# Kernel optimization log

Hardware: AMD Instinct MI355X
Metric: run time of the kernel (lower is better)

The kernel has to match this reference:

```python
import jax, jax.numpy as jnp
import numpy as np

B, S, D, L, H = 4, 2048, 1024, 2, 8  # batch, seq, d_model, hierarchy levels, heads
DH = D // H


def _ln(x, g, b, eps=1e-5):
    mu = jnp.mean(x, axis=-1, keepdims=True)
    xc = x - mu
    var = jnp.mean(xc * xc, axis=-1, keepdims=True)
    return xc * jax.lax.rsqrt(var + eps) * g + b


def setup_inputs() -> dict:
    key = jax.random.key(0)
    ks = jax.random.split(key, 16)
    s = 0.02
    f32 = jnp.float32
    return {
        "x": jax.random.normal(ks[0], (B, S, D), f32),
        "hierarchy_levels": jax.random.randint(ks[1], (B, S), 0, 3),
        # per-level processor MLPs (stacked over level axis)
        "p1_w": jax.random.normal(ks[2], (L, D, D), f32) * s,
        "p1_b": jnp.zeros((L, D), f32),
        "p2_w": jax.random.normal(ks[3], (L, D, D), f32) * s,
        "p2_b": jnp.zeros((L, D), f32),
        "ln_g": jnp.ones((L, D), f32),
        "ln_b": jnp.zeros((L, D), f32),
        # multihead attention projections
        "wq": jax.random.normal(ks[4], (D, D), f32) * s,
        "bq": jnp.zeros((D,), f32),
        "wk": jax.random.normal(ks[5], (D, D), f32) * s,
        "bk": jnp.zeros((D,), f32),
        "wv": jax.random.normal(ks[6], (D, D), f32) * s,
        "bv": jnp.zeros((D,), f32),
        "wo": jax.random.normal(ks[7], (D, D), f32) * s,
        "bo": jnp.zeros((D,), f32),
        # integration MLP: Linear(L*D -> D), SiLU, Linear(D -> D), LayerNorm
        "i1_w": jax.random.normal(ks[8], (L * D, D), f32) * s,
        "i1_b": jnp.zeros((D,), f32),
        "i2_w": jax.random.normal(ks[9], (D, D), f32) * s,
        "i2_b": jnp.zeros((D,), f32),
        "iln_g": jnp.ones((D,), f32),
        "iln_b": jnp.zeros((D,), f32),
    }


def reference(x, hierarchy_levels, p1_w, p1_b, p2_w, p2_b, ln_g, ln_b,
              wq, bq, wk, bk, wv, bv, wo, bo,
              i1_w, i1_b, i2_w, i2_b, iln_g, iln_b):
    # --- per-token expert routing: compute all L processors, select by level ---
    t = jax.nn.silu(jnp.einsum('bsd,lde->lbse', x, p1_w) + p1_b[:, None, None, :])
    h = jnp.einsum('lbse,led->lbsd', t, p2_w) + p2_b[:, None, None, :]
    h = _ln(h, ln_g[:, None, None, :], ln_b[:, None, None, :])  # [L,B,S,D]
    oh = jax.nn.one_hot(hierarchy_levels, L, dtype=x.dtype)      # [B,S,L]; level>=L -> all-zero row
    hsel = jnp.einsum('lbsd,bsl->bsd', h, oh)                    # [B,S,D]
    # --- self-attention over routed outputs ---
    q = (hsel @ wq + bq).reshape(B, S, H, DH)
    k = (hsel @ wk + bk).reshape(B, S, H, DH)
    v = (hsel @ wv + bv).reshape(B, S, H, DH)
    scores = jnp.einsum('bqhd,bkhd->bhqk', q, k) / np.sqrt(DH).astype(x.dtype)
    a = jax.nn.softmax(scores, axis=-1)                          # [B,H,S,S]
    ctx = jnp.einsum('bhqk,bkhd->bqhd', a, v).reshape(B, S, D)
    attended = ctx @ wo + bo
    attn_weights = jnp.mean(a, axis=1)                           # torch avg over heads: [B,S,S]
    # --- integration MLP ---
    z = jnp.concatenate([hsel, attended], axis=-1)               # [B,S,2D]
    z = jax.nn.silu(z @ i1_w + i1_b) @ i2_w + i2_b
    out = _ln(z, iln_g, iln_b)
    return out, attn_weights
```

## Files before the change

kernel.cpp:

```cpp
#include <hip/hip_runtime.h>
#include <cstdint>
#include <cstddef>

#define B_ 4
#define S_ 2048
#define D_ 1024
#define H_ 8
#define DH_ 128
#define MTOT 8192
#define NT_ 32
#define SCALE2 (0.08838834764831845f * 1.4426950408889634f)

typedef __attribute__((ext_vector_type(8))) short s16x8;
typedef __attribute__((ext_vector_type(4))) float f32x4;
typedef __attribute__((ext_vector_type(8))) __bf16 bf16x8;

static __device__ __forceinline__ f32x4 mfma16(s16x8 a, s16x8 b, f32x4 c) {
  return __builtin_amdgcn_mfma_f32_16x16x32_bf16(
      __builtin_bit_cast(bf16x8, a), __builtin_bit_cast(bf16x8, b), c, 0, 0, 0);
}
static __device__ __forceinline__ unsigned short f2bf(float f) {
  unsigned u = __builtin_bit_cast(unsigned, f);
  u += 0x7fffu + ((u >> 16) & 1u);
  return (unsigned short)(u >> 16);
}
static __device__ __forceinline__ unsigned cvtpk2(float a, float b) {
  unsigned r;
  asm("v_cvt_pk_bf16_f32 %0, %1, %2" : "=v"(r) : "v"(a), "v"(b));
  return r;
}
static __device__ __forceinline__ void gload_lds16(const void* g, void* l) {
  __builtin_amdgcn_global_load_lds(
      (__attribute__((address_space(1))) void*)(void*)(g),
      (__attribute__((address_space(3))) void*)(l), 16, 0, 0);
}

__global__ __launch_bounds__(256) void xconv_kernel(const float* __restrict__ x,
                                                    unsigned short* __restrict__ xb) {
  long i = ((long)blockIdx.x * 256 + threadIdx.x) * 4;
  float4 v = *(const float4*)(x + i);
  ushort4 o;
  o.x = f2bf(v.x); o.y = f2bf(v.y); o.z = f2bf(v.z); o.w = f2bf(v.w);
  *(ushort4*)(xb + i) = o;
}

__global__ __launch_bounds__(256) void route_kernel(const int* __restrict__ levels,
                                                    int* __restrict__ cnt,
                                                    int* __restrict__ ridx) {
  int row = blockIdx.x * 256 + threadIdx.x;
  int lvl = levels[row];
  if (lvl < 2) {
    int slot = atomicAdd(&cnt[lvl], 1);
    ridx[lvl * MTOT + slot] = row;
  }
}

__global__ __launch_bounds__(256) void wtrans_kernel(const float* __restrict__ in,
                                                     unsigned short* __restrict__ out,
                                                     int R, int C) {
  __shared__ unsigned short tile[32][33];
  int r0 = blockIdx.y * 32, c0 = blockIdx.x * 32;
  int tr = threadIdx.x >> 5, tc = threadIdx.x & 31;
#pragma unroll
  for (int i = 0; i < 4; i++)
    tile[tr + i * 8][tc] = f2bf(in[(long)(r0 + tr + i * 8) * C + c0 + tc]);
  __syncthreads();
#pragma unroll
  for (int i = 0; i < 4; i++)
    out[(long)(c0 + tr + i * 8) * R + r0 + tc] = tile[tc][tr + i * 8];
}

__global__ __launch_bounds__(256) void vtrans_kernel(const unsigned short* __restrict__ V,
                                                     unsigned short* __restrict__ Vt) {
  __shared__ unsigned short tile[32][33];
  int b = blockIdx.z;
  int h = blockIdx.y >> 2, d0 = (blockIdx.y & 3) * 32;
  int s0 = blockIdx.x * 32;
  int tr = threadIdx.x >> 5, tc = threadIdx.x & 31;
#pragma unroll
  for (int i = 0; i < 4; i++)
    tile[tr + i * 8][tc] = V[((long)(b * S_) + s0 + tr + i * 8) * D_ + h * DH_ + d0 + tc];
  __syncthreads();
  const int sk = s0 + tc;
  const int k6 = sk & 63;
  const int slot = ((k6 >> 5) << 5) | (((k6 >> 2) & 3) << 3) | (((k6 >> 4) & 1) << 2) | (k6 & 3);
  const int ss = (sk & ~63) | slot;
#pragma unroll
  for (int i = 0; i < 4; i++)
    Vt[((long)(b * H_ + h) * DH_ + d0 + tr + i * 8) * S_ + ss] = tile[tc][tr + i * 8];
}

template <int TAG>
__global__ __launch_bounds__(256) void gemm_kernel(
    const unsigned short* __restrict__ A, int lda,
    const unsigned short* __restrict__ Wt, int ldw,
    const float* __restrict__ bias, float oscale,
    unsigned short* __restrict__ Cb, float* __restrict__ Cf, int ldc,
    int K, int do_silu) {
  __shared__ unsigned short lA[128 * 64];
  __shared__ unsigned short lB[128 * 64];
  const int t = threadIdx.x;
  const int wid = t >> 6, lane = t & 63;
  const int g = lane >> 4, lc = lane & 15;
  const int wr = wid >> 1, wc = wid & 1;
  const int nwg = gridDim.x * gridDim.y;
  int flat = blockIdx.x + gridDim.x * blockIdx.y;
  flat = (flat & 7) * (nwg >> 3) + (flat >> 3);
  const int m0 = (flat / gridDim.x) * 128;
  const int n0 = (flat % gridDim.x) * 128;
  const int srow = lane >> 3, scol = lane & 7;
  const int sxor = (scol ^ srow) << 4;

  f32x4 acc[4][4];
#pragma unroll
  for (int i = 0; i < 4; i++)
#pragma unroll
    for (int j = 0; j < 4; j++) acc[i][j] = (f32x4){0.f, 0.f, 0.f, 0.f};

  const int nk = K >> 6;
  for (int kt = 0; kt < nk; ++kt) {
    const int k0 = kt << 6;
#pragma unroll
    for (int i = 0; i < 4; i++) {
      const int r0 = wid * 32 + i * 8;
      gload_lds16((const char*)(A + (m0 + r0 + srow) * (long)lda + k0) + sxor,
                  (char*)lA + r0 * 128);
      gload_lds16((const char*)(Wt + (n0 + r0 + srow) * (long)ldw + k0) + sxor,
                  (char*)lB + r0 * 128);
    }
    __syncthreads();
#pragma unroll
    for (int kk = 0; kk < 2; kk++) {
      s16x8 af[4], bfr[4];
#pragma unroll
      for (int i = 0; i < 4; i++) {
        int row = wr * 64 + i * 16 + lc;
        af[i] = *(const s16x8*)((const char*)lA + row * 128 +
                                ((kk * 64 + g * 16) ^ ((row & 7) << 4)));
      }
#pragma unroll
      for (int j = 0; j < 4; j++) {
        int row = wc * 64 + j * 16 + lc;
        bfr[j] = *(const s16x8*)((const char*)lB + row * 128 +
                                 ((kk * 64 + g * 16) ^ ((row & 7) << 4)));
      }
#pragma unroll
      for (int i = 0; i < 4; i++)
#pragma unroll
        for (int j = 0; j < 4; j++) acc[i][j] = mfma16(af[i], bfr[j], acc[i][j]);
    }
    __syncthreads();
  }
#pragma unroll
  for (int i = 0; i < 4; i++) {
    const long rbase = m0 + wr * 64 + i * 16 + g * 4;
#pragma unroll
    for (int j = 0; j < 4; j++) {
      const int col = n0 + wc * 64 + j * 16 + lc;
      const float bv = bias[col];
#pragma unroll
      for (int r = 0; r < 4; r++) {
        float v = (acc[i][j][r] + bv) * oscale;
        if (do_silu) v = v / (1.f + __expf(-v));
        if (Cb) Cb[(rbase + r) * (long)ldc + col] = f2bf(v);
        else Cf[(rbase + r) * (long)ldc + col] = v;
      }
    }
  }
}

template <int RMAP>
__global__ __launch_bounds__(256) void gemm_moe_kernel(
    const unsigned short* __restrict__ A, int lda,
    const unsigned short* __restrict__ Wt0, int ldw,
    const float* __restrict__ bias0,
    unsigned short* __restrict__ Cb, float* __restrict__ Cf, int ldc,
    int K, int do_silu, const int* __restrict__ ridx, const int* __restrict__ cnt2) {
  __shared__ unsigned short lA[128 * 64];
  __shared__ unsigned short lB[128 * 64];
  const int t = threadIdx.x;
  const int wid = t >> 6, lane = t & 63;
  const int g = lane >> 4, lc = lane & 15;
  const int wr = wid >> 1, wc = wid & 1;
  const int nwg = gridDim.x * gridDim.y;
  int flat = blockIdx.x + gridDim.x * blockIdx.y;
  flat = (flat & 7) * (nwg >> 3) + (flat >> 3);
  const int m0 = (flat / gridDim.x) * 128;
  const int n0 = (flat % gridDim.x) * 128;
  const int lvl = m0 >> 12;
  const int lm0 = m0 & 4095;
  if (lm0 >= cnt2[lvl]) return;
  const unsigned short* Wt = Wt0 + (long)lvl * 1048576;
  const float* bias = bias0 + lvl * 1024;
  const int srow = lane >> 3, scol = lane & 7;
  const int sxor = (scol ^ srow) << 4;

  const unsigned short* abase[4];
#pragma unroll
  for (int i = 0; i < 4; i++) {
    int ar;
    if (RMAP) ar = ridx[lvl * MTOT + lm0 + wid * 32 + i * 8 + srow];
    else ar = m0 + wid * 32 + i * 8 + srow;
    abase[i] = A + (long)ar * lda;
  }

  f32x4 acc[4][4];
#pragma unroll
  for (int i = 0; i < 4; i++)
#pragma unroll
    for (int j = 0; j < 4; j++) acc[i][j] = (f32x4){0.f, 0.f, 0.f, 0.f};

  const int nk = K >> 6;
  for (int kt = 0; kt < nk; ++kt) {
    const int k0 = kt << 6;
#pragma unroll
    for (int i = 0; i < 4; i++) {
      const int r0 = wid * 32 + i * 8;
      gload_lds16((const char*)(abase[i] + k0) + sxor, (char*)lA + r0 * 128);
      gload_lds16((const char*)(Wt + (n0 + r0 + srow) * (long)ldw + k0) + sxor,
                  (char*)lB + r0 * 128);
    }
    __syncthreads();
#pragma unroll
    for (int kk = 0; kk < 2; kk++) {
      s16x8 af[4], bfr[4];
#pragma unroll
      for (int i = 0; i < 4; i++) {
        int row = wr * 64 + i * 16 + lc;
        af[i] = *(const s16x8*)((const char*)lA + row * 128 +
                                ((kk * 64 + g * 16) ^ ((row & 7) << 4)));
      }
#pragma unroll
      for (int j = 0; j < 4; j++) {
        int row = wc * 64 + j * 16 + lc;
        bfr[j] = *(const s16x8*)((const char*)lB + row * 128 +
                                 ((kk * 64 + g * 16) ^ ((row & 7) << 4)));
      }
#pragma unroll
      for (int i = 0; i < 4; i++)
#pragma unroll
        for (int j = 0; j < 4; j++) acc[i][j] = mfma16(af[i], bfr[j], acc[i][j]);
    }
    __syncthreads();
  }
#pragma unroll
  for (int i = 0; i < 4; i++) {
    const long rbase = m0 + wr * 64 + i * 16 + g * 4;
#pragma unroll
    for (int j = 0; j < 4; j++) {
      const int col = n0 + wc * 64 + j * 16 + lc;
      const float bv = bias[col];
#pragma unroll
      for (int r = 0; r < 4; r++) {
        float v = acc[i][j][r] + bv;
        if (do_silu) v = v / (1.f + __expf(-v));
        if (Cb) Cb[(rbase + r) * (long)ldc + col] = f2bf(v);
        else Cf[(rbase + r) * (long)ldc + col] = v;
      }
    }
  }
}

__global__ __launch_bounds__(256) void ln_moe_kernel(
    const float* __restrict__ in, const int* __restrict__ ridx,
    const int* __restrict__ cnt2,
    const float* __restrict__ gg0, const float* __restrict__ bb0,
    unsigned short* __restrict__ outb, long ldo) {
  const int row = blockIdx.x;
  const int lvl = row >> 12;
  const int lrow = row & 4095;
  if (lrow >= cnt2[lvl]) return;
  const int orow = ridx[lvl * MTOT + lrow];
  const float* gg = gg0 + lvl * 1024;
  const float* bb = bb0 + lvl * 1024;
  const int t = threadIdx.x;
  const float4 v = *(const float4*)(in + (long)row * D_ + t * 4);
  float s1 = v.x + v.y + v.z + v.w;
  float s2 = v.x * v.x + v.y * v.y + v.z * v.z + v.w * v.w;
#pragma unroll
  for (int m = 32; m; m >>= 1) {
    s1 += __shfl_xor(s1, m);
    s2 += __shfl_xor(s2, m);
  }
  __shared__ float w1[4], w2[4];
  if ((t & 63) == 0) { w1[t >> 6] = s1; w2[t >> 6] = s2; }
  __syncthreads();
  s1 = w1[0] + w1[1] + w1[2] + w1[3];
  s2 = w2[0] + w2[1] + w2[2] + w2[3];
  const float mu = s1 * (1.f / D_);
  const float var = s2 * (1.f / D_) - mu * mu;
  const float rs = rsqrtf(var + 1e-5f);
#pragma unroll
  for (int jj = 0; jj < 4; jj++) {
    int col = t * 4 + jj;
    float xv = (jj == 0 ? v.x : jj == 1 ? v.y : jj == 2 ? v.z : v.w);
    float y = (xv - mu) * rs * gg[col] + bb[col];
    outb[(long)orow * ldo + col] = f2bf(y);
  }
}

__global__ __launch_bounds__(256) void ln_kernel(
    const float* __restrict__ in,
    const float* __restrict__ gg, const float* __restrict__ bb,
    float* __restrict__ outf) {
  const int row = blockIdx.x;
  const int t = threadIdx.x;
  const float4 v = *(const float4*)(in + (long)row * D_ + t * 4);
  float s1 = v.x + v.y + v.z + v.w;
  float s2 = v.x * v.x + v.y * v.y + v.z * v.z + v.w * v.w;
#pragma unroll
  for (int m = 32; m; m >>= 1) {
    s1 += __shfl_xor(s1, m);
    s2 += __shfl_xor(s2, m);
  }
  __shared__ float w1[4], w2[4];
  if ((t & 63) == 0) { w1[t >> 6] = s1; w2[t >> 6] = s2; }
  __syncthreads();
  s1 = w1[0] + w1[1] + w1[2] + w1[3];
  s2 = w2[0] + w2[1] + w2[2] + w2[3];
  const float mu = s1 * (1.f / D_);
  const float var = s2 * (1.f / D_) - mu * mu;
  const float rs = rsqrtf(var + 1e-5f);
#pragma unroll
  for (int jj = 0; jj < 4; jj++) {
    int col = t * 4 + jj;
    float xv = (jj == 0 ? v.x : jj == 1 ? v.y : jj == 2 ? v.z : v.w);
    outf[(long)row * D_ + col] = (xv - mu) * rs * gg[col] + bb[col];
  }
}

__global__ __launch_bounds__(256) void gemm_qkv_kernel(
    const unsigned short* __restrict__ A, int lda,
    const unsigned short* __restrict__ Wt,
    const float* __restrict__ bq, const float* __restrict__ bk,
    const float* __restrict__ bv,
    unsigned short* __restrict__ qb, unsigned short* __restrict__ kb,
    unsigned short* __restrict__ vb) {
  __shared__ unsigned short lA[128 * 64];
  __shared__ unsigned short lB[128 * 64];
  const int t = threadIdx.x;
  const int wid = t >> 6, lane = t & 63;
  const int g = lane >> 4, lc = lane & 15;
  const int wr = wid >> 1, wc = wid & 1;
  const int nwg = gridDim.x * gridDim.y;
  int flat = blockIdx.x + gridDim.x * blockIdx.y;
  flat = (flat & 7) * (nwg >> 3) + (flat >> 3);
  const int m0 = (flat / gridDim.x) * 128;
  const int n0 = (flat % gridDim.x) * 128;
  const int srow = lane >> 3, scol = lane & 7;
  const int sxor = (scol ^ srow) << 4;

  f32x4 acc[4][4];
#pragma unroll
  for (int i = 0; i < 4; i++)
#pragma unroll
    for (int j = 0; j < 4; j++) acc[i][j] = (f32x4){0.f, 0.f, 0.f, 0.f};

  for (int kt = 0; kt < 16; ++kt) {
    const int k0 = kt << 6;
#pragma unroll
    for (int i = 0; i < 4; i++) {
      const int r0 = wid * 32 + i * 8;
      gload_lds16((const char*)(A + (m0 + r0 + srow) * (long)lda + k0) + sxor,
                  (char*)lA + r0 * 128);
      gload_lds16((const char*)(Wt + (n0 + r0 + srow) * 1024 + k0) + sxor,
                  (char*)lB + r0 * 128);
    }
    __syncthreads();
#pragma unroll
    for (int kk = 0; kk < 2; kk++) {
      s16x8 af[4], bfr[4];
#pragma unroll
      for (int i = 0; i < 4; i++) {
        int row = wr * 64 + i * 16 + lc;
        af[i] = *(const s16x8*)((const char*)lA + row * 128 +
                                ((kk * 64 + g * 16) ^ ((row & 7) << 4)));
      }
#pragma unroll
      for (int j = 0; j < 4; j++) {
        int row = wc * 64 + j * 16 + lc;
        bfr[j] = *(const s16x8*)((const char*)lB + row * 128 +
                                 ((kk * 64 + g * 16) ^ ((row & 7) << 4)));
      }
#pragma unroll
      for (int i = 0; i < 4; i++)
#pragma unroll
        for (int j = 0; j < 4; j++) acc[i][j] = mfma16(af[i], bfr[j], acc[i][j]);
    }
    __syncthreads();
  }
  const int whichB = n0 >> 10;
  const float* bias = whichB == 0 ? bq : whichB == 1 ? bk : bv;
  unsigned short* Cb = whichB == 0 ? qb : whichB == 1 ? kb : vb;
  const float oscale = whichB == 0 ? (float)SCALE2 : 1.0f;
  const int nb = n0 & 1023;
#pragma unroll
  for (int i = 0; i < 4; i++) {
    const long rbase = m0 + wr * 64 + i * 16 + g * 4;
#pragma unroll
    for (int j = 0; j < 4; j++) {
      const int col = nb + wc * 64 + j * 16 + lc;
      const float bvv = bias[col];
#pragma unroll
      for (int r = 0; r < 4; r++) {
        float v = (acc[i][j][r] + bvv) * oscale;
        Cb[(rbase + r) * 1024L + col] = f2bf(v);
      }
    }
  }
}

__global__ __launch_bounds__(256, 2) void flash_kernel(
    const unsigned short* __restrict__ Q, const unsigned short* __restrict__ Kb,
    const unsigned short* __restrict__ Vt,
    unsigned short* __restrict__ ctx, float* __restrict__ Mo, float* __restrict__ Lo) {
  __shared__ unsigned short lK[2][64 * 128];
  __shared__ unsigned short lV[2][128 * 64];
  const int t = threadIdx.x, wid = t >> 6, lane = t & 63;
  const int g = lane >> 4, lc = lane & 15;
  const int d = blockIdx.x + 16 * (blockIdx.y + 8 * blockIdx.z);
  const int qd = d >> 3, rd = d & 7;
  const int grp = rd + 8 * (qd >> 4);
  const int b = grp >> 3, h = grp & 7, q0 = (qd & 15) * 128;
  const int k_l4 = lane >> 4, k_c = lane & 15;
  const int v_l3 = lane >> 3, v_c = lane & 7;

  s16x8 qf[2][4];
#pragma unroll
  for (int qi = 0; qi < 2; qi++)
#pragma unroll
    for (int kk = 0; kk < 4; kk++)
      qf[qi][kk] = *(const s16x8*)(Q +
          ((long)(b * S_ + q0 + wid * 32 + qi * 16 + lc)) * D_ + h * DH_ + kk * 32 + g * 8);

  f32x4 acco[2][8];
#pragma unroll
  for (int qi = 0; qi < 2; qi++)
#pragma unroll
    for (int dn = 0; dn < 8; dn++) acco[qi][dn] = (f32x4){0.f, 0.f, 0.f, 0.f};
  float m_run[2] = {-1e30f, -1e30f}, l_run[2] = {0.f, 0.f};

  auto stageK = [&](int kt, int buf) {
#pragma unroll
    for (int i = 0; i < 4; i++) {
      const int r0 = wid * 16 + i * 4;
      const int row = r0 + k_l4;
      gload_lds16((const char*)(Kb + (b * S_ + kt * 64 + row) * D_ + h * DH_) +
                      ((k_c ^ (row & 7)) << 4),
                  (char*)&lK[buf][0] + r0 * 256);
    }
  };
  auto stageV = [&](int kt, int buf) {
#pragma unroll
    for (int i = 0; i < 4; i++) {
      const int r0 = wid * 32 + i * 8;
      const int row = r0 + v_l3;
      gload_lds16((const char*)(Vt + ((b * H_ + h) * DH_ + row) * S_ + kt * 64) +
                      ((v_c ^ (row & 7)) << 4),
                  (char*)&lV[buf][0] + r0 * 128);
    }
  };

  stageK(0, 0);
  stageV(0, 0);
  __syncthreads();

  for (int kt = 0; kt < NT_; ++kt) {
    const int cur = kt & 1;
    if (kt + 1 < NT_) { stageK(kt + 1, cur ^ 1); stageV(kt + 1, cur ^ 1); }

    f32x4 s[2][4];
#pragma unroll
    for (int qi = 0; qi < 2; qi++)
#pragma unroll
      for (int kn = 0; kn < 4; kn++) s[qi][kn] = (f32x4){0.f, 0.f, 0.f, 0.f};
    __builtin_amdgcn_s_setprio(1);
#pragma unroll
    for (int kk = 0; kk < 4; kk++) {
      s16x8 kf[4];
#pragma unroll
      for (int kn = 0; kn < 4; kn++) {
        int row = kn * 16 + lc;
        kf[kn] = *(const s16x8*)((const char*)&lK[cur][0] + row * 256 +
                                 ((kk * 64 + g * 16) ^ ((row & 7) << 4)));
      }
#pragma unroll
      for (int qi = 0; qi < 2; qi++)
#pragma unroll
        for (int kn = 0; kn < 4; kn++) s[qi][kn] = mfma16(kf[kn], qf[qi][kk], s[qi][kn]);
    }
    __builtin_amdgcn_s_setprio(0);

    float mx[2];
    int trig = 0;
#pragma unroll
    for (int qi = 0; qi < 2; qi++) {
      float m01 = fmaxf(fmaxf(s[qi][0][0], s[qi][0][1]), fmaxf(s[qi][0][2], s[qi][0][3]));
      float m1 = fmaxf(fmaxf(s[qi][1][0], s[qi][1][1]), fmaxf(s[qi][1][2], s[qi][1][3]));
      float m2 = fmaxf(fmaxf(s[qi][2][0], s[qi][2][1]), fmaxf(s[qi][2][2], s[qi][2][3]));
      float m3 = fmaxf(fmaxf(s[qi][3][0], s[qi][3][1]), fmaxf(s[qi][3][2], s[qi][3][3]));
      float m = fmaxf(fmaxf(m01, m1), fmaxf(m2, m3));
      m = fmaxf(m, __shfl_xor(m, 16));
      m = fmaxf(m, __shfl_xor(m, 32));
      mx[qi] = m;
      trig |= (m > m_run[qi] + 8.0f);
    }
    if (__any(trig)) {
#pragma unroll
      for (int qi = 0; qi < 2; qi++) {
        float mn = fmaxf(m_run[qi], mx[qi]);
        float fsc = exp2f(m_run[qi] - mn);
        m_run[qi] = mn;
        l_run[qi] *= fsc;
#pragma unroll
        for (int dn = 0; dn < 8; dn++)
#pragma unroll
          for (int r = 0; r < 4; r++) acco[qi][dn][r] *= fsc;
      }
    }

    unsigned w[2][4][2];
#pragma unroll
    for (int qi = 0; qi < 2; qi++) {
      float ls = 0.f;
#pragma unroll
      for (int kn = 0; kn < 4; kn++) {
        float p0 = exp2f(s[qi][kn][0] - m_run[qi]);
        float p1 = exp2f(s[qi][kn][1] - m_run[qi]);
        float p2 = exp2f(s[qi][kn][2] - m_run[qi]);
        float p3 = exp2f(s[qi][kn][3] - m_run[qi]);
        ls += (p0 + p1) + (p2 + p3);
        w[qi][kn][0] = cvtpk2(p0, p1);
        w[qi][kn][1] = cvtpk2(p2, p3);
      }
      ls += __shfl_xor(ls, 16);
      ls += __shfl_xor(ls, 32);
      l_run[qi] += ls;
    }

    __builtin_amdgcn_s_setprio(1);
#pragma unroll
    for (int kk = 0; kk < 2; kk++) {
      s16x8 pf[2];
#pragma unroll
      for (int qi = 0; qi < 2; qi++) {
        union { unsigned u[4]; s16x8 v; } pu;
        pu.u[0] = w[qi][2 * kk][0];
        pu.u[1] = w[qi][2 * kk][1];
        pu.u[2] = w[qi][2 * kk + 1][0];
        pu.u[3] = w[qi][2 * kk + 1][1];
        pf[qi] = pu.v;
      }
#pragma unroll
      for (int dn = 0; dn < 8; dn++) {
        int vrow = dn * 16 + lc;
        s16x8 vf = *(const s16x8*)((const char*)&lV[cur][0] + vrow * 128 +
                                   ((kk * 64 + g * 16) ^ ((vrow & 7) << 4)));
#pragma unroll
        for (int qi = 0; qi < 2; qi++) acco[qi][dn] = mfma16(vf, pf[qi], acco[qi][dn]);
      }
    }
    __builtin_amdgcn_s_setprio(0);
    __syncthreads();
  }

  char* tb = (char*)&lK[0][0] + wid * 8192;
#pragma unroll
  for (int qi = 0; qi < 2; qi++) {
    float inv = 1.f / l_run[qi];
    int row = qi * 16 + lc;
#pragma unroll
    for (int dn = 0; dn < 8; dn++) {
      unsigned lo = cvtpk2(acco[qi][dn][0] * inv, acco[qi][dn][1] * inv);
      unsigned hi = cvtpk2(acco[qi][dn][2] * inv, acco[qi][dn][3] * inv);
      unsigned long long pk = (unsigned long long)lo | ((unsigned long long)hi << 32);
      *(unsigned long long*)(tb + row * 256 + ((dn * 32 + g * 8) ^ ((row & 7) << 4))) = pk;
    }
  }
  __syncthreads();
#pragma unroll
  for (int i = 0; i < 8; i++) {
    const int row = i * 4 + (lane >> 4);
    const int chunk = lane & 15;
    s16x8 vv = *(const s16x8*)(tb + row * 256 + ((chunk * 16) ^ ((row & 7) << 4)));
    *(s16x8*)(ctx + ((long)(b * S_ + q0 + wid * 32 + row)) * D_ + h * DH_ + chunk * 8) = vv;
  }
  if (g == 0) {
#pragma unroll
    for (int qi = 0; qi < 2; qi++) {
      int q = q0 + wid * 32 + qi * 16 + lc;
      Mo[(long)(b * H_ + h) * S_ + q] = m_run[qi];
      Lo[(long)(b * H_ + h) * S_ + q] = l_run[qi];
    }
  }
}

__global__ __launch_bounds__(256) void attw_kernel(
    const unsigned short* __restrict__ Q, const unsigned short* __restrict__ Kb,
    const float* __restrict__ Mo, const float* __restrict__ Lo,
    float* __restrict__ AW) {
  __shared__ unsigned short lK[2][128 * 128];
  __shared__ float lm[H_][128], winv[H_][128];
  const int t = threadIdx.x, wid = t >> 6, lane = t & 63;
  const int g = lane >> 4, lc = lane & 15;
  const int b = blockIdx.z, q0 = blockIdx.y * 128, k0 = blockIdx.x * 128;
  const int k_l4 = lane >> 4, k_c = lane & 15;

  for (int i = t; i < H_ * 128; i += 256) {
    int h = i >> 7, qq = i & 127;
    lm[h][qq] = Mo[(long)(b * H_ + h) * S_ + q0 + qq];
    winv[h][qq] = 0.125f / Lo[(long)(b * H_ + h) * S_ + q0 + qq];
  }

  auto stageK = [&](int h, int buf) {
#pragma unroll
    for (int i = 0; i < 8; i++) {
      const int r0 = wid * 32 + i * 4;
      const int row = r0 + k_l4;
      gload_lds16((const char*)(Kb + ((long)(b * S_ + k0 + row)) * D_ + h * DH_) +
                      ((k_c ^ (row & 7)) << 4),
                  (char*)&lK[buf][0] + r0 * 256);
    }
  };

  f32x4 acc[2][8];
#pragma unroll
  for (int qi = 0; qi < 2; qi++)
#pragma unroll
    for (int kn = 0; kn < 8; kn++) acc[qi][kn] = (f32x4){0.f, 0.f, 0.f, 0.f};

  stageK(0, 0);
  __syncthreads();

  for (int h = 0; h < H_; ++h) {
    const int cur = h & 1;
    if (h + 1 < H_) stageK(h + 1, cur ^ 1);
    f32x4 s[2][8];
#pragma unroll
    for (int qi = 0; qi < 2; qi++)
#pragma unroll
      for (int kn = 0; kn < 8; kn++) s[qi][kn] = (f32x4){0.f, 0.f, 0.f, 0.f};
    __builtin_amdgcn_s_setprio(1);
#pragma unroll
    for (int kk = 0; kk < 4; kk++) {
      s16x8 qa[2];
#pragma unroll
      for (int qi = 0; qi < 2; qi++)
        qa[qi] = *(const s16x8*)(Q +
            ((long)(b * S_ + q0 + wid * 32 + qi * 16 + lc)) * D_ + h * DH_ + kk * 32 + g * 8);
#pragma unroll
      for (int kn = 0; kn < 8; kn++) {
        int row = kn * 16 + lc;
        s16x8 kf = *(const s16x8*)((const char*)&lK[cur][0] + row * 256 +
                                   ((kk * 64 + g * 16) ^ ((row & 7) << 4)));
#pragma unroll
        for (int qi = 0; qi < 2; qi++) s[qi][kn] = mfma16(qa[qi], kf, s[qi][kn]);
      }
    }
    __builtin_amdgcn_s_setprio(0);
#pragma unroll
    for (int qi = 0; qi < 2; qi++)
#pragma unroll
      for (int kn = 0; kn < 8; kn++)
#pragma unroll
        for (int r = 0; r < 4; r++) {
          int qq = wid * 32 + qi * 16 + g * 4 + r;
          acc[qi][kn][r] += exp2f(s[qi][kn][r] - lm[h][qq]) * winv[h][qq];
        }
    __syncthreads();
  }
#pragma unroll
  for (int qi = 0; qi < 2; qi++)
#pragma unroll
    for (int kn = 0; kn < 8; kn++)
#pragma unroll
      for (int r = 0; r < 4; r++) {
        long q = q0 + wid * 32 + qi * 16 + g * 4 + r;
        int k = k0 + kn * 16 + lc;
        AW[((long)b * S_ + q) * S_ + k] = acc[qi][kn][r];
      }
}

__global__ void signal_kernel(float* out, float v) { out[0] = v; }

extern "C" void kernel_launch(void* const* d_in, const int* in_sizes, int n_in,
                              void* d_out, int out_size, void* d_ws, size_t ws_size,
                              hipStream_t stream) {
  constexpr size_t OFF_XB = 0;
  constexpr size_t OFF_W = 16777216ULL;
  constexpr size_t OFF_T = 39845888ULL;
  constexpr size_t OFF_HR = 56623104ULL;
  constexpr size_t OFF_Z = 90177536ULL;
  constexpr size_t OFF_Q = 123731968ULL;
  constexpr size_t OFF_K = 140509184ULL;
  constexpr size_t OFF_V = 157286400ULL;
  constexpr size_t OFF_VT = 174063616ULL;
  constexpr size_t OFF_M = 190840832ULL;
  constexpr size_t OFF_L = 191102976ULL;
  constexpr size_t OFF_CNT = 191365120ULL;
  constexpr size_t OFF_RIDX = 191365184ULL;
  constexpr size_t WS_NEED = OFF_RIDX + 2 * MTOT * 4;

  if (ws_size < WS_NEED) {
    signal_kernel<<<1, 1, 0, stream>>>((float*)d_out, (float)ws_size);
    return;
  }
  const float* x = (const float*)d_in[0];
  const int* levels = (const int*)d_in[1];
  const float* p1w = (const float*)d_in[2];
  const float* p1b = (const float*)d_in[3];
  const float* p2w = (const float*)d_in[4];
  const float* p2b = (const float*)d_in[5];
  const float* lng = (const float*)d_in[6];
  const float* lnb = (const float*)d_in[7];
  const float* wq = (const float*)d_in[8];
  const float* bq = (const float*)d_in[9];
  const float* wk = (const float*)d_in[10];
  const float* bk = (const float*)d_in[11];
  const float* wv = (const float*)d_in[12];
  const float* bv = (const float*)d_in[13];
  const float* wo = (const float*)d_in[14];
  const float* bo = (const float*)d_in[15];
  const float* i1w = (const float*)d_in[16];
  const float* i1b = (const float*)d_in[17];
  const float* i2w = (const float*)d_in[18];
  const float* i2b = (const float*)d_in[19];
  const float* ilng = (const float*)d_in[20];
  const float* ilnb = (const float*)d_in[21];

  char* ws = (char*)d_ws;
  unsigned short* xb = (unsigned short*)(ws + OFF_XB);
  unsigned short* ctx = xb;
  unsigned short* p1t = (unsigned short*)(ws + OFF_W);
  unsigned short* p2t = p1t + 2 * 1048576;
  unsigned short* wqt = p2t + 2 * 1048576;
  unsigned short* wkt = wqt + 1048576;
  unsigned short* wvt = wkt + 1048576;
  unsigned short* wot = wvt + 1048576;
  unsigned short* i1t = wot + 1048576;
  unsigned short* i2t = i1t + 2097152;
  unsigned short* tbuf = (unsigned short*)(ws + OFF_T);
  float* hraw = (float*)(ws + OFF_HR);
  unsigned short* z = (unsigned short*)(ws + OFF_Z);
  unsigned short* qb = (unsigned short*)(ws + OFF_Q);
  unsigned short* kb = (unsigned short*)(ws + OFF_K);
  unsigned short* vb = (unsigned short*)(ws + OFF_V);
  unsigned short* vt = (unsigned short*)(ws + OFF_VT);
  float* Mo = (float*)(ws + OFF_M);
  float* Lo = (float*)(ws + OFF_L);
  int* cnt = (int*)(ws + OFF_CNT);
  int* ridx = (int*)(ws + OFF_RIDX);
  float* out = (float*)d_out;
  float* aw = out + (size_t)MTOT * D_;

  dim3 blk(256);
  hipMemsetAsync(cnt, 0, 64, stream);
  hipMemsetAsync(ridx, 0, 2 * MTOT * 4, stream);
  xconv_kernel<<<8192, blk, 0, stream>>>(x, xb);
  route_kernel<<<32, blk, 0, stream>>>(levels, cnt, ridx);
  wtrans_kernel<<<dim3(32, 32), blk, 0, stream>>>(p1w, p1t, 1024, 1024);
  wtrans_kernel<<<dim3(32, 32), blk, 0, stream>>>(p1w + 1048576, p1t + 1048576, 1024, 1024);
  wtrans_kernel<<<dim3(32, 32), blk, 0, stream>>>(p2w, p2t, 1024, 1024);
  wtrans_kernel<<<dim3(32, 32), blk, 0, stream>>>(p2w + 1048576, p2t + 1048576, 1024, 1024);
  wtrans_kernel<<<dim3(32, 32), blk, 0, stream>>>(wq, wqt, 1024, 1024);
  wtrans_kernel<<<dim3(32, 32), blk, 0, stream>>>(wk, wkt, 1024, 1024);
  wtrans_kernel<<<dim3(32, 32), blk, 0, stream>>>(wv, wvt, 1024, 1024);
  wtrans_kernel<<<dim3(32, 32), blk, 0, stream>>>(wo, wot, 1024, 1024);
  wtrans_kernel<<<dim3(32, 64), blk, 0, stream>>>(i1w, i1t, 2048, 1024);
  wtrans_kernel<<<dim3(32, 32), blk, 0, stream>>>(i2w, i2t, 1024, 1024);
  hipMemsetAsync(z, 0, 33554432, stream);

  gemm_moe_kernel<1><<<dim3(8, 64), blk, 0, stream>>>(xb, 1024, p1t, 1024, p1b,
                                                      tbuf, nullptr, 1024, 1024, 1, ridx, cnt);
  gemm_moe_kernel<0><<<dim3(8, 64), blk, 0, stream>>>(tbuf, 1024, p2t, 1024, p2b,
                                                      nullptr, hraw, 1024, 1024, 0, ridx, cnt);
  ln_moe_kernel<<<8192, blk, 0, stream>>>(hraw, ridx, cnt, lng, lnb, z, 2048);

  gemm_qkv_kernel<<<dim3(24, 64), blk, 0, stream>>>(z, 2048, wqt, bq, bk, bv, qb, kb, vb);
  vtrans_kernel<<<dim3(64, 32, 4), blk, 0, stream>>>(vb, vt);
  flash_kernel<<<dim3(16, 8, 4), blk, 0, stream>>>(qb, kb, vt, ctx, Mo, Lo);
  gemm_kernel<2><<<dim3(8, 64), blk, 0, stream>>>(ctx, 1024, wot, 1024, bo, 1.0f, z + 1024,
                                                  nullptr, 2048, 1024, 0);
  attw_kernel<<<dim3(16, 16, 4), blk, 0, stream>>>(qb, kb, Mo, Lo, aw);
  gemm_kernel<3><<<dim3(8, 64), blk, 0, stream>>>(z, 2048, i1t, 2048, i1b, 1.0f, tbuf, nullptr,
                                                  1024, 2048, 1);
  gemm_kernel<4><<<dim3(8, 64), blk, 0, stream>>>(tbuf, 1024, i2t, 1024, i2b, 1.0f, nullptr,
                                                  hraw, 1024, 1024, 0);
  ln_kernel<<<8192, blk, 0, stream>>>(hraw, ilng, ilnb, out);
}
```

Baseline: 525.3 us.

## Fold output projection into integration weights and batch weight transposes

The attention output projection wo is folded algebraically into the second half of i1_w by precomputing wo·i1_w[1024:] with a small GEMM. The combined bias bo·i1_w[1024:]+i1_b is computed by its own kernel. Flash attention now writes its context straight into the z buffer, which removes the full 8192x1024x1024 out-projection GEMM from the activation path. The ten weight-transpose launches are merged into one kernel, and the attw grid is remapped for XCD locality. The cost is an extra rounding to bf16 of the fused weight product.

```diff
diff --git a/kernel.cpp b/kernel.cpp
--- a/kernel.cpp
+++ b/kernel.cpp
@@ -24,6 +24,9 @@
   u += 0x7fffu + ((u >> 16) & 1u);
   return (unsigned short)(u >> 16);
 }
+static __device__ __forceinline__ float bf2f(unsigned short u) {
+  return __builtin_bit_cast(float, (unsigned)u << 16);
+}
 static __device__ __forceinline__ unsigned cvtpk2(float a, float b) {
   unsigned r;
   asm("v_cvt_pk_bf16_f32 %0, %1, %2" : "=v"(r) : "v"(a), "v"(b));
@@ -55,19 +58,21 @@
   }
 }
 
-__global__ __launch_bounds__(256) void wtrans_kernel(const float* __restrict__ in,
-                                                     unsigned short* __restrict__ out,
-                                                     int R, int C) {
+struct WtDesc { const float* src; unsigned short* dst; long dst_ld; long dst_off; };
+struct WtArgs { WtDesc d[10]; };
+__global__ __launch_bounds__(256) void wtrans_all_kernel(WtArgs a) {
   __shared__ unsigned short tile[32][33];
-  int r0 = blockIdx.y * 32, c0 = blockIdx.x * 32;
+  const int wi = blockIdx.y >> 5;
+  const WtDesc de = a.d[wi];
+  int r0 = (blockIdx.y & 31) * 32, c0 = blockIdx.x * 32;
   int tr = threadIdx.x >> 5, tc = threadIdx.x & 31;
 #pragma unroll
   for (int i = 0; i < 4; i++)
-    tile[tr + i * 8][tc] = f2bf(in[(long)(r0 + tr + i * 8) * C + c0 + tc]);
+    tile[tr + i * 8][tc] = f2bf(de.src[(long)(r0 + tr + i * 8) * 1024 + c0 + tc]);
   __syncthreads();
 #pragma unroll
   for (int i = 0; i < 4; i++)
-    out[(long)(c0 + tr + i * 8) * R + r0 + tc] = tile[tc][tr + i * 8];
+    de.dst[(long)(c0 + tr + i * 8) * de.dst_ld + de.dst_off + r0 + tc] = tile[tc][tr + i * 8];
 }
 
 __global__ __launch_bounds__(256) void vtrans_kernel(const unsigned short* __restrict__ V,
@@ -329,6 +334,26 @@
   }
 }
 
+__global__ __launch_bounds__(256) void biascomb_kernel(
+    const unsigned short* __restrict__ i1t, const float* __restrict__ bo,
+    const float* __restrict__ i1b, float* __restrict__ bias_c) {
+  const int n = blockIdx.x * 256 + threadIdx.x;
+  float s = i1b[n];
+  for (int a0 = 0; a0 < 1024; a0 += 8) {
+    s16x8 w = *(const s16x8*)(i1t + (long)n * 2048 + 1024 + a0);
+#pragma unroll
+    for (int j = 0; j < 8; j++) s += bo[a0 + j] * bf2f((unsigned short)w[j]);
+  }
+  bias_c[n] = s;
+}
+
+__global__ __launch_bounds__(256) void copywct_kernel(
+    const unsigned short* __restrict__ wct, unsigned short* __restrict__ i1t) {
+  long idx = ((long)blockIdx.x * 256 + threadIdx.x) * 8;
+  long n = idx >> 10, c = idx & 1023;
+  *(s16x8*)(i1t + n * 2048 + 1024 + c) = *(const s16x8*)(wct + idx);
+}
+
 __global__ __launch_bounds__(256) void gemm_qkv_kernel(
     const unsigned short* __restrict__ A, int lda,
     const unsigned short* __restrict__ Wt,
@@ -413,7 +438,7 @@
 __global__ __launch_bounds__(256, 2) void flash_kernel(
     const unsigned short* __restrict__ Q, const unsigned short* __restrict__ Kb,
     const unsigned short* __restrict__ Vt,
-    unsigned short* __restrict__ ctx, float* __restrict__ Mo, float* __restrict__ Lo) {
+    unsigned short* __restrict__ zatt, float* __restrict__ Mo, float* __restrict__ Lo) {
   __shared__ unsigned short lK[2][64 * 128];
   __shared__ unsigned short lV[2][128 * 64];
   const int t = threadIdx.x, wid = t >> 6, lane = t & 63;
@@ -583,7 +608,7 @@
     const int row = i * 4 + (lane >> 4);
     const int chunk = lane & 15;
     s16x8 vv = *(const s16x8*)(tb + row * 256 + ((chunk * 16) ^ ((row & 7) << 4)));
-    *(s16x8*)(ctx + ((long)(b * S_ + q0 + wid * 32 + row)) * D_ + h * DH_ + chunk * 8) = vv;
+    *(s16x8*)(zatt + ((long)(b * S_ + q0 + wid * 32 + row)) * 2048 + h * DH_ + chunk * 8) = vv;
   }
   if (g == 0) {
 #pragma unroll
@@ -603,7 +628,10 @@
   __shared__ float lm[H_][128], winv[H_][128];
   const int t = threadIdx.x, wid = t >> 6, lane = t & 63;
   const int g = lane >> 4, lc = lane & 15;
-  const int b = blockIdx.z, q0 = blockIdx.y * 128, k0 = blockIdx.x * 128;
+  const int f = blockIdx.x + 16 * (blockIdx.y + 16 * blockIdx.z);
+  const int xcd = f & 7, i_ = f >> 3;
+  const int grp = (i_ >> 4) * 8 + xcd;
+  const int b = grp >> 4, k0 = (grp & 15) * 128, q0 = (i_ & 15) * 128;
   const int k_l4 = lane >> 4, k_c = lane & 15;
 
   for (int i = t; i < H_ * 128; i += 256) {
@@ -699,7 +727,9 @@
   constexpr size_t OFF_L = 191102976ULL;
   constexpr size_t OFF_CNT = 191365120ULL;
   constexpr size_t OFF_RIDX = 191365184ULL;
-  constexpr size_t WS_NEED = OFF_RIDX + 2 * MTOT * 4;
+  constexpr size_t OFF_BC = OFF_RIDX + 2ULL * MTOT * 4;
+  constexpr size_t OFF_ZB = OFF_BC + 4096;
+  constexpr size_t WS_NEED = OFF_ZB + 4096;
 
   if (ws_size < WS_NEED) {
     signal_kernel<<<1, 1, 0, stream>>>((float*)d_out, (float)ws_size);
@@ -730,14 +760,13 @@
 
   char* ws = (char*)d_ws;
   unsigned short* xb = (unsigned short*)(ws + OFF_XB);
-  unsigned short* ctx = xb;
   unsigned short* p1t = (unsigned short*)(ws + OFF_W);
   unsigned short* p2t = p1t + 2 * 1048576;
   unsigned short* wqt = p2t + 2 * 1048576;
   unsigned short* wkt = wqt + 1048576;
   unsigned short* wvt = wkt + 1048576;
-  unsigned short* wot = wvt + 1048576;
-  unsigned short* i1t = wot + 1048576;
+  unsigned short* wob = wvt + 1048576;
+  unsigned short* i1t = wob + 1048576;
   unsigned short* i2t = i1t + 2097152;
   unsigned short* tbuf = (unsigned short*)(ws + OFF_T);
   float* hraw = (float*)(ws + OFF_HR);
@@ -750,24 +779,35 @@
   float* Lo = (float*)(ws + OFF_L);
   int* cnt = (int*)(ws + OFF_CNT);
   int* ridx = (int*)(ws + OFF_RIDX);
+  float* bias_c = (float*)(ws + OFF_BC);
+  float* zb = (float*)(ws + OFF_ZB);
   float* out = (float*)d_out;
   float* aw = out + (size_t)MTOT * D_;
 
   dim3 blk(256);
   hipMemsetAsync(cnt, 0, 64, stream);
   hipMemsetAsync(ridx, 0, 2 * MTOT * 4, stream);
+  hipMemsetAsync(zb, 0, 4096, stream);
   xconv_kernel<<<8192, blk, 0, stream>>>(x, xb);
   route_kernel<<<32, blk, 0, stream>>>(levels, cnt, ridx);
-  wtrans_kernel<<<dim3(32, 32), blk, 0, stream>>>(p1w, p1t, 1024, 1024);
-  wtrans_kernel<<<dim3(32, 32), blk, 0, stream>>>(p1w + 1048576, p1t + 1048576, 1024, 1024);
-  wtrans_kernel<<<dim3(32, 32), blk, 0, stream>>>(p2w, p2t, 1024, 1024);
-  wtrans_kernel<<<dim3(32, 32), blk, 0, stream>>>(p2w + 1048576, p2t + 1048576, 1024, 1024);
-  wtrans_kernel<<<dim3(32, 32), blk, 0, stream>>>(wq, wqt, 1024, 1024);
-  wtrans_kernel<<<dim3(32, 32), blk, 0, stream>>>(wk, wkt, 1024, 1024);
-  wtrans_kernel<<<dim3(32, 32), blk, 0, stream>>>(wv, wvt, 1024, 1024);
-  wtrans_kernel<<<dim3(32, 32), blk, 0, stream>>>(wo, wot, 1024, 1024);
-  wtrans_kernel<<<dim3(32, 64), blk, 0, stream>>>(i1w, i1t, 2048, 1024);
-  wtrans_kernel<<<dim3(32, 32), blk, 0, stream>>>(i2w, i2t, 1024, 1024);
+
+  WtArgs wa;
+  wa.d[0] = {p1w, p1t, 1024, 0};
+  wa.d[1] = {p1w + 1048576, p1t + 1048576, 1024, 0};
+  wa.d[2] = {p2w, p2t, 1024, 0};
+  wa.d[3] = {p2w + 1048576, p2t + 1048576, 1024, 0};
+  wa.d[4] = {wq, wqt, 1024, 0};
+  wa.d[5] = {wk, wkt, 1024, 0};
+  wa.d[6] = {wv, wvt, 1024, 0};
+  wa.d[7] = {i1w, i1t, 2048, 0};
+  wa.d[8] = {i1w + 1048576, i1t, 2048, 1024};
+  wa.d[9] = {i2w, i2t, 1024, 0};
+  wtrans_all_kernel<<<dim3(32, 320), blk, 0, stream>>>(wa);
+  xconv_kernel<<<1024, blk, 0, stream>>>(wo, wob);
+  gemm_kernel<5><<<dim3(8, 8), blk, 0, stream>>>(i1t + 1024, 2048, wob, 1024, zb, 1.0f,
+                                                 tbuf, nullptr, 1024, 1024, 0);
+  biascomb_kernel<<<4, blk, 0, stream>>>(i1t, bo, i1b, bias_c);
+  copywct_kernel<<<512, blk, 0, stream>>>(tbuf, i1t);
   hipMemsetAsync(z, 0, 33554432, stream);
 
   gemm_moe_kernel<1><<<dim3(8, 64), blk, 0, stream>>>(xb, 1024, p1t, 1024, p1b,
@@ -778,12 +818,10 @@
 
   gemm_qkv_kernel<<<dim3(24, 64), blk, 0, stream>>>(z, 2048, wqt, bq, bk, bv, qb, kb, vb);
   vtrans_kernel<<<dim3(64, 32, 4), blk, 0, stream>>>(vb, vt);
-  flash_kernel<<<dim3(16, 8, 4), blk, 0, stream>>>(qb, kb, vt, ctx, Mo, Lo);
-  gemm_kernel<2><<<dim3(8, 64), blk, 0, stream>>>(ctx, 1024, wot, 1024, bo, 1.0f, z + 1024,
-                                                  nullptr, 2048, 1024, 0);
+  flash_kernel<<<dim3(16, 8, 4), blk, 0, stream>>>(qb, kb, vt, z + 1024, Mo, Lo);
   attw_kernel<<<dim3(16, 16, 4), blk, 0, stream>>>(qb, kb, Mo, Lo, aw);
-  gemm_kernel<3><<<dim3(8, 64), blk, 0, stream>>>(z, 2048, i1t, 2048, i1b, 1.0f, tbuf, nullptr,
-                                                  1024, 2048, 1);
+  gemm_kernel<3><<<dim3(8, 64), blk, 0, stream>>>(z, 2048, i1t, 2048, bias_c, 1.0f, tbuf,
+                                                  nullptr, 1024, 2048, 1);
   gemm_kernel<4><<<dim3(8, 64), blk, 0, stream>>>(tbuf, 1024, i2t, 1024, i2b, 1.0f, nullptr,
                                                   hraw, 1024, 1024, 0);
   ln_kernel<<<8192, blk, 0, stream>>>(hraw, ilng, ilnb, out);
```

New measurement: 547.0 us. +4.1%, slower.
